# Optimization experiments

Measured on AMD Instinct MI355X. Metric: run time of the kernel, lower is better.

The kernel has to match this reference:

```python
import jax, jax.numpy as jnp
import numpy as np

D_MODEL = 1024
D_STATE = 512
SEQ_LEN = 16384
R_MIN, R_MAX, MAX_PHASE = 0.0, 1.0, 6.28


def setup_inputs() -> dict:
    key = jax.random.key(0)
    ks = jax.random.split(key, 8)
    inputs = jax.random.normal(ks[0], (SEQ_LEN, D_MODEL), dtype=jnp.float32)
    # parameter init exactly as in the module
    u_nu = jax.random.uniform(ks[1], (D_STATE,), dtype=jnp.float32)
    nu_log = jnp.log(-0.5 * jnp.log(u_nu * (R_MAX ** 2 - R_MIN ** 2) + R_MIN ** 2))
    u_th = jax.random.uniform(ks[2], (D_STATE,), dtype=jnp.float32)
    theta_log = jnp.log(MAX_PHASE * u_th)
    diag_lambda = jnp.exp(-jnp.exp(nu_log) + 1j * jnp.exp(theta_log))
    gamma_log = jnp.log(jnp.sqrt(1.0 - jnp.abs(diag_lambda) ** 2))
    bn = jnp.sqrt(jnp.asarray(2 * D_MODEL, jnp.float32))
    cn = jnp.sqrt(jnp.asarray(D_STATE, jnp.float32))
    B_re = jax.random.normal(ks[3], (D_STATE, D_MODEL), dtype=jnp.float32) / bn
    B_im = jax.random.normal(ks[4], (D_STATE, D_MODEL), dtype=jnp.float32) / bn
    C_re = jax.random.normal(ks[5], (D_MODEL, D_STATE), dtype=jnp.float32) / cn
    C_im = jax.random.normal(ks[6], (D_MODEL, D_STATE), dtype=jnp.float32) / cn
    D = jax.random.normal(ks[7], (D_MODEL,), dtype=jnp.float32)
    return {"inputs": inputs, "nu_log": nu_log, "theta_log": theta_log,
            "gamma_log": gamma_log, "B_re": B_re, "B_im": B_im,
            "C_re": C_re, "C_im": C_im, "D": D}


def _binop(q_i, q_j):
    # associative combine for diagonal linear recurrence h' = a*h + b
    a_i, b_i = q_i
    a_j, b_j = q_j
    return (a_j * a_i, a_j * b_i + b_j)


def reference(inputs, nu_log, theta_log, gamma_log, B_re, B_im, C_re, C_im, D):
    L = inputs.shape[0]
    diag_lambda = jnp.exp(-jnp.exp(nu_log) + 1j * jnp.exp(theta_log))  # (d_state,)
    B_norm = (B_re + 1j * B_im) * jnp.exp(gamma_log)[:, None]          # (d_state, d_model)
    C = C_re + 1j * C_im                                               # (d_model, d_state)
    # Bu[t] = B_norm @ x_t  -> (L, d_state) complex
    Bu = inputs.astype(B_norm.dtype) @ B_norm.T
    Lambda_elems = jnp.broadcast_to(diag_lambda, (L, diag_lambda.shape[0]))
    _, h = jax.lax.associative_scan(_binop, (Lambda_elems, Bu))        # (L, d_state)
    # y_t = Re[C h_t] + D * x_t
    return jnp.real(h @ C.T) + D * inputs
```

## Files before the change

### kernel.cpp

```cpp
#include <hip/hip_runtime.h>
#include <math.h>

#define L_SEQ   16384
#define DMODEL  1024
#define NST     512
#define CHUNK   128
#define NCHUNK  (L_SEQ / CHUNK)
#define NT      16

typedef float  f32x4 __attribute__((ext_vector_type(4)));
typedef short  s16x8 __attribute__((ext_vector_type(8)));

__device__ __forceinline__ unsigned short f2bf(float f) {
    union { float f; unsigned int u; } v; v.f = f;
    unsigned int r = v.u + 0x7fffu + ((v.u >> 16) & 1u);
    return (unsigned short)(r >> 16);
}
__device__ __forceinline__ unsigned short f2bf_fast(float f) {
    union { float f; unsigned int u; } v; v.f = f;
    return (unsigned short)((v.u + 0x8000u) >> 16);
}
__device__ __forceinline__ float bf2f(unsigned int h16) {
    union { unsigned int u; float f; } v; v.u = h16 << 16; return v.f;
}
__device__ __forceinline__ void mfma16(f32x4& d, s16x8 a, s16x8 b) {
    asm volatile("v_mfma_f32_16x16x32_bf16 %0, %1, %2, %0"
                 : "+v"(d) : "v"(a), "v"(b));
}
__device__ __forceinline__ uint4 pack8(float4 x, float4 y) {
    union { unsigned short u[8]; uint4 v; } t;
    t.u[0] = f2bf_fast(x.x); t.u[1] = f2bf_fast(x.y);
    t.u[2] = f2bf_fast(x.z); t.u[3] = f2bf_fast(x.w);
    t.u[4] = f2bf_fast(y.x); t.u[5] = f2bf_fast(y.y);
    t.u[6] = f2bf_fast(y.z); t.u[7] = f2bf_fast(y.w);
    return t.v;
}
__device__ __forceinline__ void gload16(const unsigned short* g, unsigned short* l) {
    __builtin_amdgcn_global_load_lds(
        (const __attribute__((address_space(1))) unsigned int*)g,
        (__attribute__((address_space(3))) unsigned int*)l,
        16, 0, 0);
}
__device__ __forceinline__ void bar() {
    asm volatile("" ::: "memory");
    __builtin_amdgcn_s_barrier();
    asm volatile("" ::: "memory");
}

__global__ void setup_params(const float* __restrict__ nu_log,
                             const float* __restrict__ theta_log,
                             const float* __restrict__ gamma_log,
                             float* __restrict__ lam,
                             float* __restrict__ lamT,
                             float* __restrict__ gam) {
    int s = threadIdx.x;
    if (s >= NST) return;
    float mod = expf(-expf(nu_log[s]));
    float th  = expf(theta_log[s]);
    float ar = mod * cosf(th);
    float ai = mod * sinf(th);
    lam[s] = ar; lam[NST + s] = ai;
    gam[s] = expf(gamma_log[s]);
    float pr = 1.f, pi = 0.f;
    for (int i = 0; i < CHUNK; ++i) {
        float nr = pr * ar - pi * ai;
        float ni = pr * ai + pi * ar;
        pr = nr; pi = ni;
    }
    lamT[s] = pr; lamT[NST + s] = pi;
}

__global__ void pack_w1(const float* __restrict__ Bre, const float* __restrict__ Bim,
                        unsigned short* __restrict__ W1) {
    int idx = blockIdx.x * 256 + threadIdx.x;
    int n = idx >> 10, k = idx & 1023;
    int s = n >> 1;
    float v = (n & 1) ? Bim[s * DMODEL + k] : Bre[s * DMODEL + k];
    W1[idx] = f2bf(v);
}
__global__ void pack_w2(const float* __restrict__ Cre, const float* __restrict__ Cim,
                        unsigned short* __restrict__ W2) {
    int idx = blockIdx.x * 256 + threadIdx.x;
    int n = idx >> 10, k = idx & 1023;
    int s = k >> 1;
    float v = (k & 1) ? -Cim[n * NST + s] : Cre[n * NST + s];
    W2[idx] = f2bf(v);
}

__global__ __launch_bounds__(256)
void conv_x(const float4* __restrict__ X, uint4* __restrict__ Xb) {
    int i = blockIdx.x * 256 + threadIdx.x;
    float4 a = X[2 * i], b = X[2 * i + 1];
    Xb[i] = pack8(a, b);
}


#define DO_TILE(BUF, T)                                                          \
  {                                                                              \
    _Pragma("unroll")                                                            \
    for (int q = 0; q < 4; ++q) {                                                \
      if ((q & 1) == 0) {                                                        \
        _Pragma("unroll")                                                        \
        for (int i = 0; i < 4; ++i) {                                            \
          const int arow = wr * 128 + ((q >> 1) * 4 + i) * 16 + fr;              \
          _Pragma("unroll")                                                      \
          for (int kx = 0; kx < 2; ++kx)                                         \
            af[i][kx] = *(const s16x8*)                                          \
                &lds[BUF][0][arow * 64 + (((kx * 4 + g4) ^ f7) << 3)];           \
        }                                                                        \
      }                                                                          \
      s16x8 bfr[2][2];                                                           \
      _Pragma("unroll")                                                          \
      for (int j = 0; j < 2; ++j) {                                              \
        const int brow = wc * 64 + ((q & 1) * 2 + j) * 16 + fr;                  \
        _Pragma("unroll")                                                        \
        for (int kx = 0; kx < 2; ++kx)                                           \
          bfr[j][kx] = *(const s16x8*)                                           \
              &lds[BUF][1][brow * 64 + (((kx * 4 + g4) ^ f7) << 3)];             \
      }                                                                          \
      if (q == 0 && (T) + 1 < NT) {                                              \
        const size_t ksrc = (size_t)((T) + 1) * 64;                              \
        _Pragma("unroll")                                                        \
        for (int j = 0; j < 4; ++j) {                                            \
          gload16(Asrc + (size_t)(64 * j) * 1024 + ksrc,                         \
                  &lds[BUF ^ 1][0][j * 4096 + tid * 8]);                         \
          gload16(Bsrc + (size_t)(64 * j) * 1024 + ksrc,                         \
                  &lds[BUF ^ 1][1][j * 4096 + tid * 8]);                         \
        }                                                                        \
      }                                                                          \
      bar();                                                                     \
      __builtin_amdgcn_s_setprio(1);                                             \
      _Pragma("unroll")                                                          \
      for (int kx = 0; kx < 2; ++kx)                                             \
        _Pragma("unroll")                                                        \
        for (int i = 0; i < 4; ++i)                                              \
          _Pragma("unroll")                                                      \
          for (int j = 0; j < 2; ++j)                                            \
            mfma16(acc[(q >> 1) * 4 + i][(q & 1) * 2 + j], af[i][kx], bfr[j][kx]); \
      __builtin_amdgcn_s_setprio(0);                                             \
      if (q == 3) asm volatile("s_waitcnt vmcnt(0)" ::: "memory");               \
      bar();                                                                     \
    }                                                                            \
  }

template<int EPI>
__global__ __launch_bounds__(512)
void gemm_8ph(const unsigned short* __restrict__ A, const unsigned short* __restrict__ Bm,
              void* __restrict__ out, const float* __restrict__ Dv,
              const float* __restrict__ Xf) {
    __shared__ unsigned short lds[2][2][16384];

    const int tid  = threadIdx.x;
    const int lane = tid & 63;
    const int wave = tid >> 6;
    const int wr   = wave >> 2;
    const int wc   = wave & 3;
    const int fr   = lane & 15;
    const int g4   = lane >> 4;
    const int f7   = fr & 7;

    const int lin   = blockIdx.x;
    const int n_new = (lin & 7) * 32 + (lin >> 3);
    const int bx = n_new & 3, by = n_new >> 2;
    const int m0 = by * 256, n0 = bx * 256;

    const int srow_in = tid >> 3;
    const int skc     = tid & 7;
    const int kc_src  = skc ^ (srow_in & 7);
    const unsigned short* Asrc = A  + (size_t)(m0 + srow_in) * 1024 + kc_src * 8;
    const unsigned short* Bsrc = Bm + (size_t)(n0 + srow_in) * 1024 + kc_src * 8;

    f32x4 acc[8][4] = {};
    s16x8 af[4][2];

    #pragma unroll
    for (int j = 0; j < 4; ++j) {
        gload16(Asrc + (size_t)(64 * j) * 1024, &lds[0][0][j * 4096 + tid * 8]);
        gload16(Bsrc + (size_t)(64 * j) * 1024, &lds[0][1][j * 4096 + tid * 8]);
    }
    asm volatile("s_waitcnt vmcnt(0)" ::: "memory");
    bar();

    for (int tt = 0; tt < NT; tt += 2) {
        DO_TILE(0, tt)
        DO_TILE(1, tt + 1)
    }

    const int crow = (lane >> 4) * 4;
    const int ccol = lane & 15;
    #pragma unroll
    for (int mf = 0; mf < 8; ++mf) {
        #pragma unroll
        for (int j = 0; j < 4; ++j) {
            const int n  = n0 + wc * 64 + j * 16 + ccol;
            const int mb = m0 + wr * 128 + mf * 16 + crow;
            #pragma unroll
            for (int r = 0; r < 4; ++r) {
                const int m = mb + r;
                if (EPI) {
                    ((float*)out)[(size_t)m * 1024 + n] =
                        acc[mf][j][r] + Dv[n] * Xf[(size_t)m * 1024 + n];
                } else {
                    ((unsigned short*)out)[(size_t)m * 1024 + n] = f2bf(acc[mf][j][r]);
                }
            }
        }
    }
}

__global__ __launch_bounds__(128)
void scan_ends(const unsigned int* __restrict__ Bu, const float* __restrict__ lam,
               const float* __restrict__ gam, float* __restrict__ ends) {
    const int s = blockIdx.y * 128 + threadIdx.x;
    const int c = blockIdx.x;
    const float lr = lam[s], li = lam[NST + s], g = gam[s];
    float hr = 0.f, hi = 0.f;
    size_t base = (size_t)c * CHUNK * NST + s;
    #pragma unroll 4
    for (int t = 0; t < CHUNK; ++t) {
        unsigned int v = Bu[base + (size_t)t * NST];
        float br = g * bf2f(v & 0xffffu);
        float bi = g * bf2f(v >> 16);
        float nr = fmaf(lr, hr, fmaf(-li, hi, br));
        float ni = fmaf(lr, hi, fmaf( li, hr, bi));
        hr = nr; hi = ni;
    }
    ends[(size_t)(c * NST + s) * 2]     = hr;
    ends[(size_t)(c * NST + s) * 2 + 1] = hi;
}

__global__ __launch_bounds__(NST)
void scan_carry(const float* __restrict__ ends, const float* __restrict__ lamT,
                float* __restrict__ car) {
    const int s = threadIdx.x;
    const float ar = lamT[s], ai = lamT[NST + s];
    float cr = 0.f, ci = 0.f;
    for (int c = 0; c < NCHUNK; ++c) {
        car[(size_t)(c * NST + s) * 2]     = cr;
        car[(size_t)(c * NST + s) * 2 + 1] = ci;
        float er = ends[(size_t)(c * NST + s) * 2];
        float ei = ends[(size_t)(c * NST + s) * 2 + 1];
        float nr = fmaf(ar, cr, fmaf(-ai, ci, er));
        float ni = fmaf(ar, ci, fmaf( ai, cr, ei));
        cr = nr; ci = ni;
    }
}

__global__ __launch_bounds__(128)
void scan_h(const unsigned int* __restrict__ Bu, unsigned int* __restrict__ H,
            const float* __restrict__ lam, const float* __restrict__ gam,
            const float* __restrict__ car) {
    const int s = blockIdx.y * 128 + threadIdx.x;
    const int c = blockIdx.x;
    const float lr = lam[s], li = lam[NST + s], g = gam[s];
    float hr = car[(size_t)(c * NST + s) * 2];
    float hi = car[(size_t)(c * NST + s) * 2 + 1];
    size_t base = (size_t)c * CHUNK * NST + s;
    #pragma unroll 4
    for (int t = 0; t < CHUNK; ++t) {
        unsigned int v = Bu[base + (size_t)t * NST];
        float br = g * bf2f(v & 0xffffu);
        float bi = g * bf2f(v >> 16);
        float nr = fmaf(lr, hr, fmaf(-li, hi, br));
        float ni = fmaf(lr, hi, fmaf( li, hr, bi));
        hr = nr; hi = ni;
        H[base + (size_t)t * NST] =
            (unsigned int)f2bf(hr) | ((unsigned int)f2bf(hi) << 16);
    }
}

extern "C" void kernel_launch(void* const* d_in, const int* in_sizes, int n_in,
                              void* d_out, int out_size, void* d_ws, size_t ws_size,
                              hipStream_t stream) {
    const float* X         = (const float*)d_in[0];
    const float* nu_log    = (const float*)d_in[1];
    const float* theta_log = (const float*)d_in[2];
    const float* gamma_log = (const float*)d_in[3];
    const float* Bre       = (const float*)d_in[4];
    const float* Bim       = (const float*)d_in[5];
    const float* Cre       = (const float*)d_in[6];
    const float* Cim       = (const float*)d_in[7];
    const float* Dv        = (const float*)d_in[8];
    float* Y = (float*)d_out;

    char* ws = (char*)d_ws;
    size_t off = 0;
    unsigned short* Xb  = (unsigned short*)(ws + off); off += (size_t)L_SEQ * DMODEL * 2;
    unsigned short* H   = Xb;
    unsigned short* W1  = (unsigned short*)(ws + off); off += (size_t)DMODEL * DMODEL * 2;
    unsigned short* W2  = (unsigned short*)(ws + off); off += (size_t)DMODEL * DMODEL * 2;
    float* lam  = (float*)(ws + off); off += 1024 * 4;
    float* lamT = (float*)(ws + off); off += 1024 * 4;
    float* gam  = (float*)(ws + off); off += 512 * 4;
    float* ends = (float*)(ws + off); off += (size_t)NCHUNK * NST * 2 * 4;
    float* car  = (float*)(ws + off); off += (size_t)NCHUNK * NST * 2 * 4;
    unsigned short* Bu = (unsigned short*)d_out;

    setup_params<<<1, NST, 0, stream>>>(nu_log, theta_log, gamma_log, lam, lamT, gam);
    pack_w1<<<(DMODEL * DMODEL) / 256, 256, 0, stream>>>(Bre, Bim, W1);
    pack_w2<<<(DMODEL * DMODEL) / 256, 256, 0, stream>>>(Cre, Cim, W2);
    conv_x<<<(L_SEQ * DMODEL / 8) / 256, 256, 0, stream>>>((const float4*)X, (uint4*)Xb);

    gemm_8ph<0><<<256, 512, 0, stream>>>(Xb, W1, Bu, nullptr, nullptr);

    dim3 gs(NCHUNK, 4);
    scan_ends<<<gs, 128, 0, stream>>>((const unsigned int*)Bu, lam, gam, ends);
    scan_carry<<<1, NST, 0, stream>>>(ends, lamT, car);
    scan_h<<<gs, 128, 0, stream>>>((const unsigned int*)Bu, (unsigned int*)H, lam, gam, car);

    gemm_8ph<1><<<256, 512, 0, stream>>>(H, W2, Y, Dv, X);
}
```

Baseline: 170.0 us.

## Restructure GEMM into finer-grained multi-stage LDS pipeline with k-major layout

Replaces the per-tile double-buffered load of full A/B tiles with a finer pipeline that issues four smaller half-K stages (A/B × two k-halves) spread across the four compute phases, waiting with partial vmcnt instead of draining every tile. The LDS layout changes from row-major swizzled to a k-group-major layout so fragment reads need no XOR swizzle. The aim is to keep more global loads in flight and overlap them more evenly with MFMA work. The risk is more LDS bank conflicts from the new layout and fragile vmcnt bookkeeping.

```diff
diff --git a/kernel.cpp b/kernel.cpp
--- a/kernel.cpp
+++ b/kernel.cpp
@@ -95,60 +95,44 @@
 }
 
 
-#define DO_TILE(BUF, T)                                                          \
-  {                                                                              \
-    _Pragma("unroll")                                                            \
-    for (int q = 0; q < 4; ++q) {                                                \
-      if ((q & 1) == 0) {                                                        \
-        _Pragma("unroll")                                                        \
-        for (int i = 0; i < 4; ++i) {                                            \
-          const int arow = wr * 128 + ((q >> 1) * 4 + i) * 16 + fr;              \
-          _Pragma("unroll")                                                      \
-          for (int kx = 0; kx < 2; ++kx)                                         \
-            af[i][kx] = *(const s16x8*)                                          \
-                &lds[BUF][0][arow * 64 + (((kx * 4 + g4) ^ f7) << 3)];           \
-        }                                                                        \
-      }                                                                          \
-      s16x8 bfr[2][2];                                                           \
-      _Pragma("unroll")                                                          \
-      for (int j = 0; j < 2; ++j) {                                              \
-        const int brow = wc * 64 + ((q & 1) * 2 + j) * 16 + fr;                  \
-        _Pragma("unroll")                                                        \
-        for (int kx = 0; kx < 2; ++kx)                                           \
-          bfr[j][kx] = *(const s16x8*)                                           \
-              &lds[BUF][1][brow * 64 + (((kx * 4 + g4) ^ f7) << 3)];             \
-      }                                                                          \
-      if (q == 0 && (T) + 1 < NT) {                                              \
-        const size_t ksrc = (size_t)((T) + 1) * 64;                              \
-        _Pragma("unroll")                                                        \
-        for (int j = 0; j < 4; ++j) {                                            \
-          gload16(Asrc + (size_t)(64 * j) * 1024 + ksrc,                         \
-                  &lds[BUF ^ 1][0][j * 4096 + tid * 8]);                         \
-          gload16(Bsrc + (size_t)(64 * j) * 1024 + ksrc,                         \
-                  &lds[BUF ^ 1][1][j * 4096 + tid * 8]);                         \
-        }                                                                        \
-      }                                                                          \
-      bar();                                                                     \
-      __builtin_amdgcn_s_setprio(1);                                             \
-      _Pragma("unroll")                                                          \
-      for (int kx = 0; kx < 2; ++kx)                                             \
-        _Pragma("unroll")                                                        \
-        for (int i = 0; i < 4; ++i)                                              \
-          _Pragma("unroll")                                                      \
-          for (int j = 0; j < 2; ++j)                                            \
-            mfma16(acc[(q >> 1) * 4 + i][(q & 1) * 2 + j], af[i][kx], bfr[j][kx]); \
-      __builtin_amdgcn_s_setprio(0);                                             \
-      if (q == 3) asm volatile("s_waitcnt vmcnt(0)" ::: "memory");               \
-      bar();                                                                     \
-    }                                                                            \
+#define STAGE(BUF, OP, KX, T) do {                                              \
+    const unsigned short* s_ = ((OP) ? Bsrc : Asrc) + (size_t)(T) * 64 + (KX) * 32; \
+    gload16(s_,      &lds[BUF][(OP) * 2 + (KX)][tid * 8]);                      \
+    gload16(s_ + 16, &lds[BUF][(OP) * 2 + (KX)][4096 + tid * 8]);               \
+} while (0)
+
+#define PH(BUF, Q, STG, GATE)                                                   \
+  {                                                                             \
+    if (((Q) & 1) == 0) {                                                       \
+      _Pragma("unroll")                                                         \
+      for (int m = 0; m < 8; ++m)                                               \
+        af[m] = *(const s16x8*)&lds[BUF][(Q) >> 1]                              \
+                 [g4 * 2048 + (wr * 128 + m * 16 + fr) * 8];                    \
+    }                                                                           \
+    s16x8 bfr[2];                                                               \
+    _Pragma("unroll")                                                           \
+    for (int j = 0; j < 2; ++j)                                                 \
+      bfr[j] = *(const s16x8*)&lds[BUF][2 + ((Q) >> 1)]                         \
+                [g4 * 2048 + (wc * 64 + ((Q) & 1) * 32 + j * 16 + fr) * 8];     \
+    STG;                                                                        \
+    bar();                                                                      \
+    __builtin_amdgcn_s_setprio(1);                                              \
+    _Pragma("unroll")                                                           \
+    for (int m = 0; m < 8; ++m) {                                               \
+      mfma16(acc[m][((Q) & 1) * 2 + 0], af[m], bfr[0]);                         \
+      mfma16(acc[m][((Q) & 1) * 2 + 1], af[m], bfr[1]);                         \
+    }                                                                           \
+    __builtin_amdgcn_s_setprio(0);                                              \
+    GATE;                                                                       \
+    bar();                                                                      \
   }
 
 template<int EPI>
 __global__ __launch_bounds__(512)
-void gemm_8ph(const unsigned short* __restrict__ A, const unsigned short* __restrict__ Bm,
-              void* __restrict__ out, const float* __restrict__ Dv,
-              const float* __restrict__ Xf) {
-    __shared__ unsigned short lds[2][2][16384];
+void gemm_pipe(const unsigned short* __restrict__ A, const unsigned short* __restrict__ Bm,
+               void* __restrict__ out, const float* __restrict__ Dv,
+               const float* __restrict__ Xf) {
+    __shared__ __align__(16) unsigned short lds[2][4][8192];
 
     const int tid  = threadIdx.x;
     const int lane = tid & 63;
@@ -157,33 +141,31 @@
     const int wc   = wave & 3;
     const int fr   = lane & 15;
     const int g4   = lane >> 4;
-    const int f7   = fr & 7;
 
     const int lin   = blockIdx.x;
     const int n_new = (lin & 7) * 32 + (lin >> 3);
     const int bx = n_new & 3, by = n_new >> 2;
     const int m0 = by * 256, n0 = bx * 256;
 
-    const int srow_in = tid >> 3;
-    const int skc     = tid & 7;
-    const int kc_src  = skc ^ (srow_in & 7);
-    const unsigned short* Asrc = A  + (size_t)(m0 + srow_in) * 1024 + kc_src * 8;
-    const unsigned short* Bsrc = Bm + (size_t)(n0 + srow_in) * 1024 + kc_src * 8;
+    const unsigned short* Asrc = A  + (size_t)(m0 + (tid & 255)) * 1024 + (tid >> 8) * 8;
+    const unsigned short* Bsrc = Bm + (size_t)(n0 + (tid & 255)) * 1024 + (tid >> 8) * 8;
 
     f32x4 acc[8][4] = {};
-    s16x8 af[4][2];
-
-    #pragma unroll
-    for (int j = 0; j < 4; ++j) {
-        gload16(Asrc + (size_t)(64 * j) * 1024, &lds[0][0][j * 4096 + tid * 8]);
-        gload16(Bsrc + (size_t)(64 * j) * 1024, &lds[0][1][j * 4096 + tid * 8]);
-    }
-    asm volatile("s_waitcnt vmcnt(0)" ::: "memory");
+    s16x8 af[8];
+
+    STAGE(0, 0, 0, 0); STAGE(0, 1, 0, 0); STAGE(0, 0, 1, 0); STAGE(0, 1, 1, 0);
+    STAGE(1, 0, 0, 1); STAGE(1, 1, 0, 1); STAGE(1, 0, 1, 1);
+    asm volatile("s_waitcnt vmcnt(6)" ::: "memory");
     bar();
 
-    for (int tt = 0; tt < NT; tt += 2) {
-        DO_TILE(0, tt)
-        DO_TILE(1, tt + 1)
+    for (int t = 0; t < NT; ++t) {
+        const int bb = t & 1;
+        PH(bb, 0, { if (t + 1 < NT) STAGE(bb ^ 1, 1, 1, t + 1); }, {})
+        PH(bb, 1, { if (t + 2 < NT) STAGE(bb, 0, 0, t + 2); }, {})
+        PH(bb, 2, { if (t + 2 < NT) STAGE(bb, 1, 0, t + 2); }, {})
+        PH(bb, 3, { if (t + 2 < NT) STAGE(bb, 0, 1, t + 2); },
+           { if (t < NT - 2)       asm volatile("s_waitcnt vmcnt(6)" ::: "memory");
+             else if (t == NT - 2) asm volatile("s_waitcnt vmcnt(0)" ::: "memory"); })
     }
 
     const int crow = (lane >> 4) * 4;
@@ -301,12 +283,12 @@
     pack_w2<<<(DMODEL * DMODEL) / 256, 256, 0, stream>>>(Cre, Cim, W2);
     conv_x<<<(L_SEQ * DMODEL / 8) / 256, 256, 0, stream>>>((const float4*)X, (uint4*)Xb);
 
-    gemm_8ph<0><<<256, 512, 0, stream>>>(Xb, W1, Bu, nullptr, nullptr);
+    gemm_pipe<0><<<256, 512, 0, stream>>>(Xb, W1, Bu, nullptr, nullptr);
 
     dim3 gs(NCHUNK, 4);
     scan_ends<<<gs, 128, 0, stream>>>((const unsigned int*)Bu, lam, gam, ends);
     scan_carry<<<1, NST, 0, stream>>>(ends, lamT, car);
     scan_h<<<gs, 128, 0, stream>>>((const unsigned int*)Bu, (unsigned int*)H, lam, gam, car);
 
-    gemm_8ph<1><<<256, 512, 0, stream>>>(H, W2, Y, Dv, X);
-}
+    gemm_pipe<1><<<256, 512, 0, stream>>>(H, W2, Y, Dv, X);
+}
```

After: 195.4 us. +15.0%, slower.
